# Kernel tuning notes

Hardware: AMD Instinct MI355X
Metric: run time of the kernel (lower is better)

## Reference

```python
import jax, jax.numpy as jnp
import numpy as np


def setup_inputs() -> dict:
    key = jax.random.key(0)
    ks = jax.random.split(key, 16)
    B, D, H = 65536, 64, 512
    s = 0.05
    inp = {
        "state": jax.random.normal(ks[0], (B, D), dtype=jnp.float32),
        "Wz0": jax.random.normal(ks[1], (H, D), dtype=jnp.float32) * s,
        "bz0": jax.random.normal(ks[2], (H,), dtype=jnp.float32) * s,
        "Wz1": jax.random.normal(ks[3], (H, H), dtype=jnp.float32) * s,
        "Wz2": jax.random.normal(ks[4], (H, H), dtype=jnp.float32) * s,
        "Wz3": jax.random.normal(ks[5], (H, H), dtype=jnp.float32) * s,
        "WzL": jax.random.normal(ks[6], (1, H), dtype=jnp.float32) * s,
        "Wx0": jax.random.normal(ks[7], (H, D), dtype=jnp.float32) * s,
        "bx0": jax.random.normal(ks[8], (H,), dtype=jnp.float32) * s,
        "Wx1": jax.random.normal(ks[9], (H, D), dtype=jnp.float32) * s,
        "bx1": jax.random.normal(ks[10], (H,), dtype=jnp.float32) * s,
        "Wx2": jax.random.normal(ks[11], (H, D), dtype=jnp.float32) * s,
        "bx2": jax.random.normal(ks[12], (H,), dtype=jnp.float32) * s,
        "WxL": jax.random.normal(ks[13], (1, D), dtype=jnp.float32) * s,
    }
    return inp


def reference(state, Wz0, bz0, Wz1, Wz2, Wz3, WzL, Wx0, bx0, Wx1, bx1, Wx2, bx2, WxL):
    sp = jax.nn.softplus

    def icnn_sum(x):  # x: [B, D] -> scalar (sum of per-sample convex outputs)
        z = sp(x @ Wz0.T + bz0)                      # [B, H]
        z = sp(z @ Wz1.T + x @ Wx0.T + bx0)          # [B, H]
        z = sp(z @ Wz2.T + x @ Wx1.T + bx1)          # [B, H]
        z = sp(z @ Wz3.T + x @ Wx2.T + bx2)          # [B, H]
        out = z @ WzL.T + x @ WxL.T                  # [B, 1]
        return out.sum()

    x = state - 1.0
    # Output is scalar per-sample, so grad of the batch-sum equals the stacked
    # per-sample jacobians computed by the torch Python loop.
    action = jax.grad(icnn_sum)(x)                   # [B, D]
    return action
```

## Files before the change

### kernel.cpp

```cpp
#include <hip/hip_runtime.h>

typedef unsigned short u16;
typedef unsigned int u32;
typedef unsigned long long u64;

#define B_TOTAL 65536
#define H 512
#define D 64
#define BM 64

typedef __bf16 bf16x8 __attribute__((ext_vector_type(8)));
typedef float f32x4 __attribute__((ext_vector_type(4)));

__device__ __forceinline__ u32 f2b(float f) {
  u32 u = __builtin_bit_cast(u32, f);
  return (u + 0x7fffu + ((u >> 16) & 1u)) >> 16;
}
__device__ __forceinline__ float b2f(u32 bits) {
  return __builtin_bit_cast(float, bits << 16);
}

#define OFF_Wz0b 0
#define OFF_Wx0b 32768
#define OFF_Wx1b 65536
#define OFF_Wx2b 98304
#define OFF_Wz1b 131072
#define OFF_Wz2b 393216
#define OFF_Wz3b 655360
#define OFF_Wz1t 917504
#define OFF_Wz2t 1179648
#define OFF_Wz3t 1441792
#define OFF_Wz0t 1703936
#define OFF_Wx0t 1736704
#define OFF_Wx1t 1769472
#define OFF_Wx2t 1802240
#define OFF_WEND 1835008
#define SLAB_ELEMS (B_TOTAL * H)
#define OFF_S0 OFF_WEND
#define OFF_S1 (OFF_S0 + SLAB_ELEMS)
#define OFF_S2 (OFF_S1 + SLAB_ELEMS)
#define WS_ELEMS (OFF_S2 + SLAB_ELEMS)

__global__ __launch_bounds__(256) void prep_kernel(
    const float* __restrict__ Wz0, const float* __restrict__ Wz1,
    const float* __restrict__ Wz2, const float* __restrict__ Wz3,
    const float* __restrict__ Wx0, const float* __restrict__ Wx1,
    const float* __restrict__ Wx2, u16* __restrict__ wsb) {
  int i = blockIdx.x * 256 + threadIdx.x;
  const float* src;
  int NN, KK, trans, p;
  if (i < 131072) {
    int r = i >> 15; p = i & 32767;
    src = (r == 0) ? Wz0 : (r == 1) ? Wx0 : (r == 2) ? Wx1 : Wx2;
    NN = 512; KK = 64; trans = 0;
  } else if (i < 917504) {
    int j = i - 131072; int r = j >> 18; p = j & 262143;
    src = (r == 0) ? Wz1 : (r == 1) ? Wz2 : Wz3;
    NN = 512; KK = 512; trans = 0;
  } else if (i < 1703936) {
    int j = i - 917504; int r = j >> 18; p = j & 262143;
    src = (r == 0) ? Wz1 : (r == 1) ? Wz2 : Wz3;
    NN = 512; KK = 512; trans = 1;
  } else {
    int j = i - 1703936; int r = j >> 15; p = j & 32767;
    src = (r == 0) ? Wz0 : (r == 1) ? Wx0 : (r == 2) ? Wx1 : Wx2;
    NN = 64; KK = 512; trans = 1;
  }
  int jj = p & 7, lane = (p >> 3) & 63, blk = p >> 9;
  int kt_sh = (KK == 64) ? 1 : 4;
  int ntile = blk >> kt_sh;
  int kstep = blk & ((1 << kt_sh) - 1);
  int n = ntile * 16 + (lane & 15);
  int k = kstep * 32 + ((lane >> 4) << 3) + jj;
  float v = trans ? src[k * NN + n] : src[n * KK + k];
  wsb[i] = (u16)f2b(v);
}

__global__ __launch_bounds__(256) void fill_sentinel(float* out, int n) {
  int i = blockIdx.x * 256 + threadIdx.x;
  if (i < n) out[i] = 12345.0f;
}

__global__ __launch_bounds__(512, 2) void icnn_kernel(
    const float* __restrict__ state,
    const float* __restrict__ bz0, const float* __restrict__ bx0,
    const float* __restrict__ bx1, const float* __restrict__ bx2,
    const float* __restrict__ WzL, const float* __restrict__ WxL,
    u16* __restrict__ wsw, float* __restrict__ out) {
  __shared__ u16 zbuf[BM * H];
  __shared__ u16 wbuf[2 * 16384];
  __shared__ f32x4 park[16 * 64];
  u16* xbuf = (u16*)park;

  const int tid = threadIdx.x;
  const int w = tid >> 6;
  const int lane = tid & 63;
  const int l15 = lane & 15;
  const int q = lane >> 4;
  const int blk = blockIdx.x;

  const u16* Wz0b = wsw + OFF_Wz0b;
  const u16* Wx0b = wsw + OFF_Wx0b;
  const u16* Wx1b = wsw + OFF_Wx1b;
  const u16* Wx2b = wsw + OFF_Wx2b;
  const u16* Wz1b = wsw + OFF_Wz1b;
  const u16* Wz2b = wsw + OFF_Wz2b;
  const u16* Wz3b = wsw + OFF_Wz3b;
  const u16* Wz1t = wsw + OFF_Wz1t;
  const u16* Wz2t = wsw + OFF_Wz2t;
  const u16* Wz3t = wsw + OFF_Wz3t;
  const u16* Wz0t = wsw + OFF_Wz0t;
  const u16* Wx0t = wsw + OFF_Wx0t;
  const u16* Wx1t = wsw + OFF_Wx1t;
  const u16* Wx2t = wsw + OFF_Wx2t;
  u64* slab0 = (u64*)(wsw + OFF_S0);
  u64* slab1 = (u64*)(wsw + OFF_S1);
  u64* slab2 = (u64*)(wsw + OFF_S2);

  {
    int r = tid >> 3, c0 = (tid & 7) << 3;
    const float* p = state + (blk * BM + r) * D + c0;
    f32x4 v0 = __builtin_nontemporal_load((const f32x4*)p);
    f32x4 v1 = __builtin_nontemporal_load((const f32x4*)(p + 4));
    u32* dst = (u32*)&xbuf[r * 72 + c0];
    dst[0] = f2b(v0[0] - 1.0f) | (f2b(v0[1] - 1.0f) << 16);
    dst[1] = f2b(v0[2] - 1.0f) | (f2b(v0[3] - 1.0f) << 16);
    dst[2] = f2b(v1[0] - 1.0f) | (f2b(v1[1] - 1.0f) << 16);
    dst[3] = f2b(v1[2] - 1.0f) | (f2b(v1[3] - 1.0f) << 16);
  }

  f32x4 acc[4][4];
  const f32x4 Z = {0.f, 0.f, 0.f, 0.f};

  auto ldA = [&](int mt, int step) -> bf16x8 {
    int m = mt * 16 + l15;
    int idx = m * H + (((step * 4 + q) ^ (m & 7)) << 3);
    return *(const bf16x8*)(&zbuf[idx]);
  };
  auto ldX = [&](int mt, int ks) -> bf16x8 {
    return *(const bf16x8*)(&xbuf[(mt * 16 + l15) * 72 + ks * 32 + q * 8]);
  };
  auto wrZ = [&](int row, int n, u16 bits) {
    zbuf[row * H + ((((n >> 3) ^ (row & 7))) << 3) + (n & 7)] = bits;
  };

  auto stageW = [&](const u16* Wp, int st, int buf) {
    const u16* gb = Wp + (w * 4 * 16 + st) * 512 + lane * 8;
    u16* lb = &wbuf[buf * 16384 + (w * 4) * 512];
#pragma unroll
    for (int j = 0; j < 4; ++j)
      __builtin_amdgcn_global_load_lds(
          (const __attribute__((address_space(1))) void*)(gb + j * 16 * 512),
          (__attribute__((address_space(3))) void*)(lb + j * 512), 16, 0, 0);
  };

  auto fwdX = [&](const u16* Wxp, bool zero_first) {
    const u16* xb = Wxp + lane * 8;
#pragma unroll
    for (int ks = 0; ks < 2; ++ks) {
      bf16x8 ax[4];
#pragma unroll
      for (int mt = 0; mt < 4; ++mt) ax[mt] = ldX(mt, ks);
      bf16x8 b4[4];
#pragma unroll
      for (int nt = 0; nt < 4; ++nt)
        b4[nt] = *(const bf16x8*)(xb + ((w * 4 + nt) * 2 + ks) * 512);
#pragma unroll
      for (int nt = 0; nt < 4; ++nt)
#pragma unroll
        for (int mt = 0; mt < 4; ++mt) {
          f32x4 c = (zero_first && ks == 0) ? Z : acc[mt][nt];
          acc[mt][nt] = __builtin_amdgcn_mfma_f32_16x16x32_bf16(ax[mt], b4[nt], c, 0, 0, 0);
        }
    }
  };

  auto fwdH = [&](const u16* Wp) {
#pragma unroll
    for (int st = 0; st < 16; ++st) {
      if (st < 15) {
        stageW(Wp, st + 1, (st + 1) & 1);
        asm volatile("s_waitcnt vmcnt(4)" ::: "memory");
      } else {
        asm volatile("s_waitcnt vmcnt(0)" ::: "memory");
      }
      const u16* wb = &wbuf[(st & 1) * 16384 + (w * 4) * 512 + lane * 8];
      bf16x8 a[4];
#pragma unroll
      for (int mt = 0; mt < 4; ++mt) a[mt] = ldA(mt, st);
#pragma unroll
      for (int nt = 0; nt < 4; ++nt) {
        bf16x8 b = *(const bf16x8*)(wb + nt * 512);
#pragma unroll
        for (int mt = 0; mt < 4; ++mt)
          acc[mt][nt] = __builtin_amdgcn_mfma_f32_16x16x32_bf16(
              a[mt], b, (st == 0) ? Z : acc[mt][nt], 0, 0, 0);
      }
    }
  };

  auto fwd_epi = [&](const float* biasp, u64* slab) {
    float bias[4];
#pragma unroll
    for (int nt = 0; nt < 4; ++nt) bias[nt] = biasp[(w * 4 + nt) * 16 + l15];
#pragma unroll
    for (int mt = 0; mt < 4; ++mt)
#pragma unroll
      for (int nt = 0; nt < 4; ++nt) {
        int n = (w * 4 + nt) * 16 + l15;
        f32x4 A = acc[mt][nt];
        u64 pack = 0;
#pragma unroll
        for (int r = 0; r < 4; ++r) {
          float a = A[r] + bias[nt];
          float t = __expf(-a);
          float u = 1.0f + t;
          float s = __builtin_amdgcn_rcpf(u);
          float z = a + __logf(u);
          pack |= (u64)f2b(s) << (16 * r);
          wrZ(mt * 16 + q * 4 + r, n, (u16)f2b(z));
        }
        slab[((blk * 8 + w) * 16 + mt * 4 + nt) * 64 + lane] = pack;
      }
  };
  auto d3_epi = [&](const float* biasp) {
    float bias[4], wl[4];
#pragma unroll
    for (int nt = 0; nt < 4; ++nt) {
      bias[nt] = biasp[(w * 4 + nt) * 16 + l15];
      wl[nt] = WzL[(w * 4 + nt) * 16 + l15];
    }
#pragma unroll
    for (int mt = 0; mt < 4; ++mt)
#pragma unroll
      for (int nt = 0; nt < 4; ++nt) {
        int n = (w * 4 + nt) * 16 + l15;
        f32x4 A = acc[mt][nt];
#pragma unroll
        for (int r = 0; r < 4; ++r) {
          float a = A[r] + bias[nt];
          float t = __expf(-a);
          float s = __builtin_amdgcn_rcpf(1.0f + t);
          wrZ(mt * 16 + q * 4 + r, n, (u16)f2b(wl[nt] * s));
        }
      }
  };
  auto bwd_epi = [&](const u64* slab) {
    u64 v[4][4];
#pragma unroll
    for (int mt = 0; mt < 4; ++mt)
#pragma unroll
      for (int nt = 0; nt < 4; ++nt)
        v[mt][nt] = slab[((blk * 8 + w) * 16 + mt * 4 + nt) * 64 + lane];
#pragma unroll
    for (int mt = 0; mt < 4; ++mt)
#pragma unroll
      for (int nt = 0; nt < 4; ++nt) {
        int n = (w * 4 + nt) * 16 + l15;
        f32x4 A = acc[mt][nt];
#pragma unroll
        for (int r = 0; r < 4; ++r) {
          float s = b2f((u32)(v[mt][nt] >> (16 * r)) & 0xffffu);
          wrZ(mt * 16 + q * 4 + r, n, (u16)f2b(A[r] * s));
        }
      }
  };

  auto minigrad = [&](const u16* Wg, bool init) {
    int mt = w & 3, c0 = w >> 2;
    bf16x8 g0[16], g1[16];
#pragma unroll
    for (int st = 0; st < 16; ++st)
      g0[st] = *(const bf16x8*)(Wg + (c0 * 16 + st) * 512 + lane * 8);
#pragma unroll
    for (int st = 0; st < 16; ++st)
      g1[st] = *(const bf16x8*)(Wg + ((c0 + 2) * 16 + st) * 512 + lane * 8);
    f32x4 t0 = Z, t1 = Z;
#pragma unroll
    for (int st = 0; st < 16; ++st) {
      bf16x8 a = ldA(mt, st);
      t0 = __builtin_amdgcn_mfma_f32_16x16x32_bf16(a, g0[st], t0, 0, 0, 0);
      t1 = __builtin_amdgcn_mfma_f32_16x16x32_bf16(a, g1[st], t1, 0, 0, 0);
    }
    if (init) {
      park[w * 64 + lane] = t0;
      park[(w + 8) * 64 + lane] = t1;
    } else {
      park[w * 64 + lane] += t0;
      park[(w + 8) * 64 + lane] += t1;
    }
  };

  __syncthreads();
  fwdX(Wz0b, true);
  stageW(Wz1b, 0, 0);
  fwd_epi(bz0, slab0);
  __syncthreads();
  fwdH(Wz1b); fwdX(Wx0b, false);
  __syncthreads();
  stageW(Wz2b, 0, 0);
  fwd_epi(bx0, slab1);
  __syncthreads();
  fwdH(Wz2b); fwdX(Wx1b, false);
  __syncthreads();
  stageW(Wz3b, 0, 0);
  fwd_epi(bx1, slab2);
  __syncthreads();
  fwdH(Wz3b); fwdX(Wx2b, false);
  __syncthreads();
  stageW(Wz3t, 0, 0);
  d3_epi(bx2);
  __syncthreads();
  minigrad(Wx2t, true);
  fwdH(Wz3t);
  __syncthreads();
  stageW(Wz2t, 0, 0);
  bwd_epi(slab2);
  __syncthreads();
  minigrad(Wx1t, false);
  fwdH(Wz2t);
  __syncthreads();
  stageW(Wz1t, 0, 0);
  bwd_epi(slab1);
  __syncthreads();
  minigrad(Wx0t, false);
  fwdH(Wz1t);
  __syncthreads();
  bwd_epi(slab0);
  __syncthreads();
  {
    int mt = w & 3, c0 = w >> 2;
    bf16x8 g0[16], g1[16];
#pragma unroll
    for (int st = 0; st < 16; ++st)
      g0[st] = *(const bf16x8*)(Wz0t + (c0 * 16 + st) * 512 + lane * 8);
#pragma unroll
    for (int st = 0; st < 16; ++st)
      g1[st] = *(const bf16x8*)(Wz0t + ((c0 + 2) * 16 + st) * 512 + lane * 8);
    f32x4 t0 = Z, t1 = Z;
#pragma unroll
    for (int st = 0; st < 16; ++st) {
      bf16x8 a = ldA(mt, st);
      t0 = __builtin_amdgcn_mfma_f32_16x16x32_bf16(a, g0[st], t0, 0, 0, 0);
      t1 = __builtin_amdgcn_mfma_f32_16x16x32_bf16(a, g1[st], t1, 0, 0, 0);
    }
    f32x4 p0 = park[w * 64 + lane];
    f32x4 p1 = park[(w + 8) * 64 + lane];
    float wx0 = WxL[c0 * 16 + l15];
    float wx1 = WxL[(c0 + 2) * 16 + l15];
#pragma unroll
    for (int r = 0; r < 4; ++r) {
      int row = blk * BM + mt * 16 + q * 4 + r;
      out[row * D + c0 * 16 + l15] = t0[r] + p0[r] + wx0;
      out[row * D + (c0 + 2) * 16 + l15] = t1[r] + p1[r] + wx1;
    }
  }
}

extern "C" void kernel_launch(void* const* d_in, const int* in_sizes, int n_in,
                              void* d_out, int out_size, void* d_ws, size_t ws_size,
                              hipStream_t stream) {
  const float* state = (const float*)d_in[0];
  const float* Wz0 = (const float*)d_in[1];
  const float* bz0 = (const float*)d_in[2];
  const float* Wz1 = (const float*)d_in[3];
  const float* Wz2 = (const float*)d_in[4];
  const float* Wz3 = (const float*)d_in[5];
  const float* WzL = (const float*)d_in[6];
  const float* Wx0 = (const float*)d_in[7];
  const float* bx0 = (const float*)d_in[8];
  const float* Wx1 = (const float*)d_in[9];
  const float* bx1 = (const float*)d_in[10];
  const float* Wx2 = (const float*)d_in[11];
  const float* bx2 = (const float*)d_in[12];
  const float* WxL = (const float*)d_in[13];

  if (ws_size < (size_t)WS_ELEMS * 2) {
    fill_sentinel<<<(out_size + 255) / 256, 256, 0, stream>>>((float*)d_out, out_size);
    return;
  }
  u16* wsw = (u16*)d_ws;
  prep_kernel<<<OFF_WEND / 256, 256, 0, stream>>>(Wz0, Wz1, Wz2, Wz3, Wx0, Wx1, Wx2, wsw);
  icnn_kernel<<<B_TOTAL / BM, 512, 0, stream>>>(state, bz0, bx0, bx1, bx2, WzL, WxL,
                                                wsw, (float*)d_out);
}
```

Baseline: 494.6 us.

## Drop LDS weight staging, read weights from global, raise occupancy to 4 blocks

```diff
diff --git a/kernel.cpp b/kernel.cpp
--- a/kernel.cpp
+++ b/kernel.cpp
@@ -81,16 +81,14 @@
   if (i < n) out[i] = 12345.0f;
 }
 
-__global__ __launch_bounds__(512, 2) void icnn_kernel(
+__global__ __launch_bounds__(512, 4) void icnn_kernel(
     const float* __restrict__ state,
     const float* __restrict__ bz0, const float* __restrict__ bx0,
     const float* __restrict__ bx1, const float* __restrict__ bx2,
     const float* __restrict__ WzL, const float* __restrict__ WxL,
     u16* __restrict__ wsw, float* __restrict__ out) {
   __shared__ u16 zbuf[BM * H];
-  __shared__ u16 wbuf[2 * 16384];
-  __shared__ f32x4 park[16 * 64];
-  u16* xbuf = (u16*)park;
+  __shared__ u16 xbuf[BM * 72];
 
   const int tid = threadIdx.x;
   const int w = tid >> 6;
@@ -131,6 +129,7 @@
 
   f32x4 acc[4][4];
   const f32x4 Z = {0.f, 0.f, 0.f, 0.f};
+  f32x4 p0 = Z, p1 = Z;
 
   auto ldA = [&](int mt, int step) -> bf16x8 {
     int m = mt * 16 + l15;
@@ -144,16 +143,6 @@
     zbuf[row * H + ((((n >> 3) ^ (row & 7))) << 3) + (n & 7)] = bits;
   };
 
-  auto stageW = [&](const u16* Wp, int st, int buf) {
-    const u16* gb = Wp + (w * 4 * 16 + st) * 512 + lane * 8;
-    u16* lb = &wbuf[buf * 16384 + (w * 4) * 512];
-#pragma unroll
-    for (int j = 0; j < 4; ++j)
-      __builtin_amdgcn_global_load_lds(
-          (const __attribute__((address_space(1))) void*)(gb + j * 16 * 512),
-          (__attribute__((address_space(3))) void*)(lb + j * 512), 16, 0, 0);
-  };
-
   auto fwdX = [&](const u16* Wxp, bool zero_first) {
     const u16* xb = Wxp + lane * 8;
 #pragma unroll
@@ -176,21 +165,15 @@
   };
 
   auto fwdH = [&](const u16* Wp) {
+    const u16* wb = Wp + (w * 4 * 16) * 512 + lane * 8;
 #pragma unroll
     for (int st = 0; st < 16; ++st) {
-      if (st < 15) {
-        stageW(Wp, st + 1, (st + 1) & 1);
-        asm volatile("s_waitcnt vmcnt(4)" ::: "memory");
-      } else {
-        asm volatile("s_waitcnt vmcnt(0)" ::: "memory");
-      }
-      const u16* wb = &wbuf[(st & 1) * 16384 + (w * 4) * 512 + lane * 8];
       bf16x8 a[4];
 #pragma unroll
       for (int mt = 0; mt < 4; ++mt) a[mt] = ldA(mt, st);
 #pragma unroll
       for (int nt = 0; nt < 4; ++nt) {
-        bf16x8 b = *(const bf16x8*)(wb + nt * 512);
+        bf16x8 b = *(const bf16x8*)(wb + (nt * 16 + st) * 512);
 #pragma unroll
         for (int mt = 0; mt < 4; ++mt)
           acc[mt][nt] = __builtin_amdgcn_mfma_f32_16x16x32_bf16(
@@ -220,7 +203,8 @@
           pack |= (u64)f2b(s) << (16 * r);
           wrZ(mt * 16 + q * 4 + r, n, (u16)f2b(z));
         }
-        slab[((blk * 8 + w) * 16 + mt * 4 + nt) * 64 + lane] = pack;
+        __builtin_nontemporal_store(
+            pack, &slab[((blk * 8 + w) * 16 + mt * 4 + nt) * 64 + lane]);
       }
   };
   auto d3_epi = [&](const float* biasp) {
@@ -251,7 +235,8 @@
     for (int mt = 0; mt < 4; ++mt)
 #pragma unroll
       for (int nt = 0; nt < 4; ++nt)
-        v[mt][nt] = slab[((blk * 8 + w) * 16 + mt * 4 + nt) * 64 + lane];
+        v[mt][nt] = __builtin_nontemporal_load(
+            &slab[((blk * 8 + w) * 16 + mt * 4 + nt) * 64 + lane]);
 #pragma unroll
     for (int mt = 0; mt < 4; ++mt)
 #pragma unroll
@@ -266,93 +251,62 @@
       }
   };
 
-  auto minigrad = [&](const u16* Wg, bool init) {
+  auto minigrad = [&](const u16* Wg) {
     int mt = w & 3, c0 = w >> 2;
-    bf16x8 g0[16], g1[16];
-#pragma unroll
-    for (int st = 0; st < 16; ++st)
-      g0[st] = *(const bf16x8*)(Wg + (c0 * 16 + st) * 512 + lane * 8);
-#pragma unroll
-    for (int st = 0; st < 16; ++st)
-      g1[st] = *(const bf16x8*)(Wg + ((c0 + 2) * 16 + st) * 512 + lane * 8);
-    f32x4 t0 = Z, t1 = Z;
+    const u16* gb = Wg + lane * 8;
+    f32x4 t0 = p0, t1 = p1;
 #pragma unroll
     for (int st = 0; st < 16; ++st) {
       bf16x8 a = ldA(mt, st);
-      t0 = __builtin_amdgcn_mfma_f32_16x16x32_bf16(a, g0[st], t0, 0, 0, 0);
-      t1 = __builtin_amdgcn_mfma_f32_16x16x32_bf16(a, g1[st], t1, 0, 0, 0);
-    }
-    if (init) {
-      park[w * 64 + lane] = t0;
-      park[(w + 8) * 64 + lane] = t1;
-    } else {
-      park[w * 64 + lane] += t0;
-      park[(w + 8) * 64 + lane] += t1;
-    }
+      bf16x8 g0 = *(const bf16x8*)(gb + (c0 * 16 + st) * 512);
+      bf16x8 g1 = *(const bf16x8*)(gb + ((c0 + 2) * 16 + st) * 512);
+      t0 = __builtin_amdgcn_mfma_f32_16x16x32_bf16(a, g0, t0, 0, 0, 0);
+      t1 = __builtin_amdgcn_mfma_f32_16x16x32_bf16(a, g1, t1, 0, 0, 0);
+    }
+    p0 = t0; p1 = t1;
   };
 
   __syncthreads();
   fwdX(Wz0b, true);
-  stageW(Wz1b, 0, 0);
   fwd_epi(bz0, slab0);
   __syncthreads();
   fwdH(Wz1b); fwdX(Wx0b, false);
   __syncthreads();
-  stageW(Wz2b, 0, 0);
   fwd_epi(bx0, slab1);
   __syncthreads();
   fwdH(Wz2b); fwdX(Wx1b, false);
   __syncthreads();
-  stageW(Wz3b, 0, 0);
   fwd_epi(bx1, slab2);
   __syncthreads();
   fwdH(Wz3b); fwdX(Wx2b, false);
   __syncthreads();
-  stageW(Wz3t, 0, 0);
   d3_epi(bx2);
   __syncthreads();
-  minigrad(Wx2t, true);
+  minigrad(Wx2t);
   fwdH(Wz3t);
   __syncthreads();
-  stageW(Wz2t, 0, 0);
   bwd_epi(slab2);
   __syncthreads();
-  minigrad(Wx1t, false);
+  minigrad(Wx1t);
   fwdH(Wz2t);
   __syncthreads();
-  stageW(Wz1t, 0, 0);
   bwd_epi(slab1);
   __syncthreads();
-  minigrad(Wx0t, false);
+  minigrad(Wx0t);
   fwdH(Wz1t);
   __syncthreads();
   bwd_epi(slab0);
   __syncthreads();
+  minigrad(Wz0t);
   {
     int mt = w & 3, c0 = w >> 2;
-    bf16x8 g0[16], g1[16];
-#pragma unroll
-    for (int st = 0; st < 16; ++st)
-      g0[st] = *(const bf16x8*)(Wz0t + (c0 * 16 + st) * 512 + lane * 8);
-#pragma unroll
-    for (int st = 0; st < 16; ++st)
-      g1[st] = *(const bf16x8*)(Wz0t + ((c0 + 2) * 16 + st) * 512 + lane * 8);
-    f32x4 t0 = Z, t1 = Z;
-#pragma unroll
-    for (int st = 0; st < 16; ++st) {
-      bf16x8 a = ldA(mt, st);
-      t0 = __builtin_amdgcn_mfma_f32_16x16x32_bf16(a, g0[st], t0, 0, 0, 0);
-      t1 = __builtin_amdgcn_mfma_f32_16x16x32_bf16(a, g1[st], t1, 0, 0, 0);
-    }
-    f32x4 p0 = park[w * 64 + lane];
-    f32x4 p1 = park[(w + 8) * 64 + lane];
     float wx0 = WxL[c0 * 16 + l15];
     float wx1 = WxL[(c0 + 2) * 16 + l15];
 #pragma unroll
     for (int r = 0; r < 4; ++r) {
       int row = blk * BM + mt * 16 + q * 4 + r;
-      out[row * D + c0 * 16 + l15] = t0[r] + p0[r] + wx0;
-      out[row * D + (c0 + 2) * 16 + l15] = t1[r] + p1[r] + wx1;
+      __builtin_nontemporal_store(p0[r] + wx0, &out[row * D + c0 * 16 + l15]);
+      __builtin_nontemporal_store(p1[r] + wx1, &out[row * D + (c0 + 2) * 16 + l15]);
     }
   }
 }
```

Measured after the change: 1.020 ms. 106% more time.
